# Kernel tuning notes

Measured on AMD Instinct MI355X. Metric: run time of the kernel, lower is better.

## Reference

```python
import jax, jax.numpy as jnp
import numpy as np

NUM_GRAPHS = 1024  # static number of segments for global_mean_pool


def setup_inputs() -> dict:
    key = jax.random.key(0)
    ks = jax.random.split(key, 16)
    N, E, F_IN, H = 100000, 1000000, 32, 64
    NUM_ATOM, NUM_ACT, L = 16, 8, 3
    s = 0.05
    x = jax.random.normal(ks[0], (N, F_IN), dtype=jnp.float32)
    edge_index = jax.random.randint(ks[1], (2, E), 0, N, dtype=jnp.int64)
    batch = jnp.sort(jax.random.randint(ks[2], (N,), 0, NUM_GRAPHS, dtype=jnp.int64))
    W_emb = jax.random.normal(ks[3], (F_IN, H), dtype=jnp.float32) * s
    b_emb = jnp.zeros((H,), dtype=jnp.float32)
    W_convs = jax.random.normal(ks[4], (L, H, H), dtype=jnp.float32) * s
    b_convs = jnp.zeros((L, H), dtype=jnp.float32)
    W_act = jax.random.normal(ks[5], (H, NUM_ACT), dtype=jnp.float32) * s
    b_act = jnp.zeros((NUM_ACT,), dtype=jnp.float32)
    W_tgt = jax.random.normal(ks[6], (H, 1), dtype=jnp.float32) * s
    b_tgt = jnp.zeros((1,), dtype=jnp.float32)
    W_atom = jax.random.normal(ks[7], (H, NUM_ATOM), dtype=jnp.float32) * s
    b_atom = jnp.zeros((NUM_ATOM,), dtype=jnp.float32)
    return {"x": x, "edge_index": edge_index, "batch": batch,
            "W_emb": W_emb, "b_emb": b_emb, "W_convs": W_convs, "b_convs": b_convs,
            "W_act": W_act, "b_act": b_act, "W_tgt": W_tgt, "b_tgt": b_tgt,
            "W_atom": W_atom, "b_atom": b_atom}


def reference(x, edge_index, batch, W_emb, b_emb, W_convs, b_convs,
              W_act, b_act, W_tgt, b_tgt, W_atom, b_atom):
    N = x.shape[0]
    # --- GCN normalization with self-loops (PyG GCNConv default) ---
    self_idx = jnp.arange(N, dtype=edge_index.dtype)
    src = jnp.concatenate([edge_index[0], self_idx])  # message source (row)
    dst = jnp.concatenate([edge_index[1], self_idx])  # aggregation target (col)
    ones_e = jnp.ones(src.shape[0], dtype=x.dtype)
    deg = jax.ops.segment_sum(ones_e, dst, num_segments=N)  # in-degree + self-loop
    dinv = jnp.where(deg > 0, jax.lax.rsqrt(deg), 0.0)
    norm = (dinv[src] * dinv[dst])[:, None]  # [E+N, 1]

    h = jax.nn.relu(x @ W_emb + b_emb)  # node embedding
    for i in range(W_convs.shape[0]):
        m = (h @ W_convs[i])[src] * norm            # gather + scale
        agg = jax.ops.segment_sum(m, dst, num_segments=N)  # scatter-add
        h = jax.nn.relu(agg + b_convs[i])

    # --- global mean pool over graphs ---
    cnt = jax.ops.segment_sum(jnp.ones(N, dtype=x.dtype), batch, num_segments=NUM_GRAPHS)
    pooled = jax.ops.segment_sum(h, batch, num_segments=NUM_GRAPHS)
    pooled = pooled / jnp.maximum(cnt, 1.0)[:, None]

    action_type_logits = pooled @ W_act + b_act            # [G, num_action_types]
    target_node_logits = (h @ W_tgt + b_tgt)[:, 0]         # [N]
    new_atom_type_logits = pooled @ W_atom + b_atom        # [G, num_atom_types]
    return (action_type_logits, target_node_logits, new_atom_type_logits, h)
```

## Files before the change

kernel.cpp:

```cpp
#include <hip/hip_runtime.h>
#include <hip/hip_fp16.h>

#define HD 64
#define FIN 32
#define NG 1024
#define STRIDE 64
#define SLOT0 4
#define DEGCAP 59
#define SH 72

#define BINW 128
#define NBMAX 1024
#define EPB 8192
#define BINCAP 2048

typedef _Float16 f16x8 __attribute__((ext_vector_type(8)));
typedef float f32x4 __attribute__((ext_vector_type(4)));
typedef int i32x4 __attribute__((ext_vector_type(4)));

__device__ __forceinline__ int fmap(int jt, int c) {
    return (jt < 2) ? (2 * c + jt) : (32 + 2 * c + (jt - 2));
}

__device__ __forceinline__ void nt_store_h2(__half2 v, __half2* p) {
    __builtin_nontemporal_store(*(int*)&v, (int*)p);
}

__global__ __launch_bounds__(256) void k_prep(const int* __restrict__ dst,
                                              int* __restrict__ blkHist,
                                              int E, int NBINS,
                                              __half2* __restrict__ BaZR,
                                              __half2* __restrict__ BbZR,
                                              const float* __restrict__ Wconv,
                                              __half* __restrict__ Wf, int wtotal,
                                              const float* __restrict__ Wemb,
                                              __half* __restrict__ Wef) {
    __shared__ int hist[NBMAX];
    int b = blockIdx.x, t = threadIdx.x;
    if (b < 48) {
        int tid = b * 256 + t;
        if (tid < wtotal) {
            int layer = tid >> 12;
            int r = tid & 4095;
            int frag = r >> 9, lane = (r >> 3) & 63, e = r & 7;
            int jt = frag >> 1, kh = frag & 1;
            int k = kh * 32 + (lane >> 4) * 8 + e;
            int n = fmap(jt, lane & 15);
            Wf[tid] = (_Float16)Wconv[(size_t)layer * 4096 + k * 64 + n];
        }
    } else if (b < 56) {
        int tid = (b - 48) * 256 + t;
        if (tid < 2048) {
            int jt = tid >> 9, lane = (tid >> 3) & 63, e = tid & 7;
            int k = (lane >> 4) * 8 + e;
            int n = fmap(jt, lane & 15);
            Wef[tid] = (_Float16)Wemb[k * HD + n];
        }
    } else if (b == 56) {
        __half2 z = __floats2half2_rn(0.f, 0.f);
        if (t < 32) BaZR[t] = z;
        else if (t < 64) BbZR[t - 32] = z;
    }
    int e0 = b * EPB;
    if (e0 < E) {
        for (int i = t; i < NBMAX; i += 256) hist[i] = 0;
        __syncthreads();
        int e1 = e0 + EPB; if (e1 > E) e1 = E;
        for (int e = e0 + t; e < e1; e += 256) atomicAdd(&hist[dst[e] >> 7], 1);
        __syncthreads();
        for (int i = t; i < NBINS; i += 256) blkHist[b * NBMAX + i] = hist[i];
    }
}

__global__ __launch_bounds__(256) void k_scanA(int* __restrict__ blkHist,
                                               int* __restrict__ binTot, int nb) {
    __shared__ int s[256];
    int i = blockIdx.x;
    int t = threadIdx.x;
    int x = (t < nb) ? blkHist[t * NBMAX + i] : 0;
    s[t] = x;
    __syncthreads();
    for (int off = 1; off < 256; off <<= 1) {
        int v = s[t];
        int u = (t >= off) ? s[t - off] : 0;
        __syncthreads();
        s[t] = v + u;
        __syncthreads();
    }
    if (t < nb) blkHist[t * NBMAX + i] = s[t] - x;
    if (t == 255) binTot[i] = s[255];
}

__global__ __launch_bounds__(256) void k_scatter(const int* __restrict__ src,
                                                 const int* __restrict__ dst,
                                                 const int* __restrict__ blkBase,
                                                 int* __restrict__ binned,
                                                 int E, int NBINS) {
    __shared__ int base[NBMAX];
    __shared__ int lpos[NBMAX];
    int b = blockIdx.x, t = threadIdx.x;
    for (int i = t; i < NBMAX; i += 256) {
        lpos[i] = 0;
        base[i] = (i < NBINS) ? blkBase[b * NBMAX + i] : 0;
    }
    __syncthreads();
    int e0 = b * EPB;
    int e1 = e0 + EPB; if (e1 > E) e1 = E;
    for (int e = e0 + t; e < e1; e += 256) {
        int d = dst[e];
        int bin = d >> 7;
        int off = base[bin] + atomicAdd(&lpos[bin], 1);
        if (off < BINCAP)
            binned[bin * BINCAP + off] = (src[e] << 7) | (d & (BINW - 1));
    }
}

__global__ __launch_bounds__(256) void k_csr(const int* __restrict__ binned,
                                             const int* __restrict__ binTot,
                                             int* __restrict__ col, int N) {
    __shared__ int img[BINW * 64];
    __shared__ int cnt[BINW];
    int b = blockIdx.x, t = threadIdx.x;
    for (int i = t; i < BINW; i += 256) cnt[i] = 0;
    __syncthreads();
    int s = b * BINCAP;
    int tot = binTot[b]; if (tot > BINCAP) tot = BINCAP;
    int e = s + tot;
    for (int i = s + t; i < e; i += 256) {
        int w = binned[i];
        int ld = w & (BINW - 1);
        int p = atomicAdd(&cnt[ld], 1);
        if (p < STRIDE - SLOT0) img[ld * 64 + SLOT0 + p] = (int)((unsigned)w >> 7);
    }
    __syncthreads();
    for (int i = t; i < BINW; i += 256) img[i * 64] = cnt[i];
    __syncthreads();
    int v0 = b * BINW;
    int* out = col + ((size_t)v0 << 6);
    for (int j = t; j < BINW * 16; j += 256) {
        int row = j >> 4, j16 = j & 15;
        int node = v0 + row;
        int deg = cnt[row]; if (deg > DEGCAP) deg = DEGCAP;
        bool keep = (j16 == 0) || (j16 <= ((deg + 3) >> 2));
        if (node < N && keep) {
            i32x4 val = *(i32x4*)&img[j * 4];
            __builtin_nontemporal_store(val, (i32x4*)(out + j * 4));
        }
    }
}

__device__ __forceinline__ void gemm_from_lds(const __half* hs, const float* dvs,
                                              const float4* __restrict__ Wf4,
                                              __half2* __restrict__ Bout,
                                              int node0, int N, int t) {
    int lane = t & 63;
    int wv = t >> 6;
    int lm = lane & 15, kq = lane >> 4;
    union U { float4 f; f16x8 h; };
    U a0, a1;
    const __half* hrow = hs + (size_t)(wv * 16 + lm) * SH;
    a0.f = *(const float4*)(hrow + kq * 8);
    a1.f = *(const float4*)(hrow + 32 + kq * 8);
    f32x4 acc[4];
#pragma unroll
    for (int jt = 0; jt < 4; jt++) acc[jt] = (f32x4){0.f, 0.f, 0.f, 0.f};
#pragma unroll
    for (int jt = 0; jt < 4; jt++) {
        U b0, b1;
        b0.f = Wf4[(jt * 2 + 0) * 64 + lane];
        b1.f = Wf4[(jt * 2 + 1) * 64 + lane];
        acc[jt] = __builtin_amdgcn_mfma_f32_16x16x32_f16(a0.h, b0.h, acc[jt], 0, 0, 0);
        acc[jt] = __builtin_amdgcn_mfma_f32_16x16x32_f16(a1.h, b1.h, acc[jt], 0, 0, 0);
    }
#pragma unroll
    for (int r = 0; r < 4; r++) {
        int lv = wv * 16 + kq * 4 + r;
        int v = node0 + lv;
        if (v < N) {
            float dv = dvs[lv];
            nt_store_h2(__floats2half2_rn(acc[0][r] * dv, acc[1][r] * dv),
                        Bout + (size_t)v * 32 + lm);
            nt_store_h2(__floats2half2_rn(acc[2][r] * dv, acc[3][r] * dv),
                        Bout + (size_t)v * 32 + 16 + lm);
        }
    }
}

__global__ __launch_bounds__(256) void k_emb_gemm0(const float* __restrict__ x,
                                                   const float4* __restrict__ Wef4,
                                                   const float* __restrict__ bemb,
                                                   const int* __restrict__ col,
                                                   const float4* __restrict__ Wf0,
                                                   __half2* __restrict__ Bout, int N) {
    __shared__ __half hs[64 * SH];
    __shared__ float dvs[64];
    int t = threadIdx.x;
    int lane = t & 63;
    int wv = t >> 6;
    int node0 = blockIdx.x * 64;
    int nodew = node0 + wv * 16;
    int m = lane & 15, kq = lane >> 4;

    int vm = nodew + m;
    if (vm > N - 1) vm = N - 1;
    const float4* xr = (const float4*)(x + (size_t)vm * FIN + kq * 8);
    float4 xa = xr[0], xb = xr[1];
    f16x8 a;
    a[0] = (_Float16)xa.x; a[1] = (_Float16)xa.y; a[2] = (_Float16)xa.z; a[3] = (_Float16)xa.w;
    a[4] = (_Float16)xb.x; a[5] = (_Float16)xb.y; a[6] = (_Float16)xb.z; a[7] = (_Float16)xb.w;

    union U { float4 f; f16x8 h; };
    f32x4 acc[4];
#pragma unroll
    for (int jt = 0; jt < 4; jt++) {
        U b; b.f = Wef4[jt * 64 + lane];
        acc[jt] = (f32x4){0.f, 0.f, 0.f, 0.f};
        acc[jt] = __builtin_amdgcn_mfma_f32_16x16x32_f16(a, b.h, acc[jt], 0, 0, 0);
    }
    float b01x = bemb[2 * m], b01y = bemb[2 * m + 1];
    float b23x = bemb[32 + 2 * m], b23y = bemb[32 + 2 * m + 1];
    __half2 z = __floats2half2_rn(0.f, 0.f);
#pragma unroll
    for (int r = 0; r < 4; r++) {
        int lv = wv * 16 + kq * 4 + r;
        int v = node0 + lv;
        __half2 p01 = z, p23 = z;
        if (v < N) {
            p01 = __floats2half2_rn(fmaxf(acc[0][r] + b01x, 0.f),
                                    fmaxf(acc[1][r] + b01y, 0.f));
            p23 = __floats2half2_rn(fmaxf(acc[2][r] + b23x, 0.f),
                                    fmaxf(acc[3][r] + b23y, 0.f));
        }
        *(__half2*)(hs + (size_t)lv * SH + 2 * m) = p01;
        *(__half2*)(hs + (size_t)lv * SH + 32 + 2 * m) = p23;
        if (m == 0)
            dvs[lv] = (v < N) ? rsqrtf((float)(col[(size_t)v << 6] + 1)) : 1.f;
    }
    __syncthreads();
    gemm_from_lds(hs, dvs, Wf0, Bout, node0, N, t);
}

__global__ __launch_bounds__(256) void k_layer(const __half2* __restrict__ Bin,
                                               const int* __restrict__ col,
                                               const float* __restrict__ bias,
                                               const float4* __restrict__ Wnext,
                                               __half2* __restrict__ Bout,
                                               int N, int ZR) {
    __shared__ __half hs[64 * SH];
    __shared__ float dvs[64];
    int t = threadIdx.x;
    int lane = t & 63;
    int wv = t >> 6;
    int node0 = blockIdx.x * 64;
    int q = lane >> 4, p = lane & 15;
    float4 b4 = *(const float4*)(bias + 4 * p);

#pragma unroll
    for (int pass = 0; pass < 4; pass++) {
        int lv = wv * 16 + pass * 4 + q;
        int v = node0 + lv;
        int vc = (v < N) ? v : 0;
        const int* bucket = col + ((size_t)vc << 6);
        int degraw = bucket[0];
        int deg = degraw > DEGCAP ? DEGCAP : degraw;
        int dmax = deg;
        dmax = max(dmax, __shfl_xor(dmax, 16, 64));
        dmax = max(dmax, __shfl_xor(dmax, 32, 64));
        int rounds = (dmax + 4) >> 2;

        float2 a0 = make_float2(0.f, 0.f), a1 = make_float2(0.f, 0.f);
        for (int rd = 0; rd < rounds; rd++) {
            int4 iq = *(const int4*)(bucket + SLOT0 + rd * 4);
            int idx[4] = {iq.x, iq.y, iq.z, iq.w};
#pragma unroll
            for (int r = 0; r < 4; r++) {
                int i = rd * 4 + r;
                idx[r] = (i < deg) ? idx[r] : ((i == deg) ? vc : ZR);
            }
            float2 raw[4];
#pragma unroll
            for (int r = 0; r < 4; r++)
                raw[r] = *(const float2*)(Bin + (size_t)idx[r] * 32 + p * 2);
#pragma unroll
            for (int r = 0; r < 4; r++) {
                float2 f0 = __half22float2(((const __half2*)&raw[r])[0]);
                float2 f1 = __half22float2(((const __half2*)&raw[r])[1]);
                a0.x += f0.x; a0.y += f0.y; a1.x += f1.x; a1.y += f1.y;
            }
        }
        float dv = rsqrtf((float)(degraw + 1));
        float r0 = fmaxf(dv * a0.x + b4.x, 0.f);
        float r1 = fmaxf(dv * a0.y + b4.y, 0.f);
        float r2 = fmaxf(dv * a1.x + b4.z, 0.f);
        float r3 = fmaxf(dv * a1.y + b4.w, 0.f);
        if (v >= N) { r0 = r1 = r2 = r3 = 0.f; dv = 1.f; }
        __half* hrow = hs + (size_t)lv * SH + 4 * p;
        *(__half2*)(hrow) = __floats2half2_rn(r0, r1);
        *(__half2*)(hrow + 2) = __floats2half2_rn(r2, r3);
        if (p == 0) dvs[lv] = dv;
    }
    __syncthreads();
    gemm_from_lds(hs, dvs, Wnext, Bout, node0, N, t);
}

__global__ __launch_bounds__(256) void k_gather_last(const __half2* __restrict__ Bin,
                                                     const int* __restrict__ col,
                                                     const float* __restrict__ bias,
                                                     float* __restrict__ hout,
                                                     const float* __restrict__ Wtgt,
                                                     const float* __restrict__ btgt,
                                                     float* __restrict__ tgt,
                                                     int N, int ZR) {
    int t = threadIdx.x;
    int lane = t & 63;
    int wv = t >> 6;
    int q = lane >> 4, p = lane & 15;
    int v = blockIdx.x * 16 + wv * 4 + q;
    if (v >= N) return;

    const int* bucket = col + ((size_t)v << 6);
    int degraw = bucket[0];
    int deg = degraw > DEGCAP ? DEGCAP : degraw;
    int dmax = deg;
    dmax = max(dmax, __shfl_xor(dmax, 16, 64));
    dmax = max(dmax, __shfl_xor(dmax, 32, 64));
    int rounds = (dmax + 4) >> 2;

    float2 a0 = make_float2(0.f, 0.f), a1 = make_float2(0.f, 0.f);
    for (int rd = 0; rd < rounds; rd++) {
        int4 iq = *(const int4*)(bucket + SLOT0 + rd * 4);
        int idx[4] = {iq.x, iq.y, iq.z, iq.w};
#pragma unroll
        for (int r = 0; r < 4; r++) {
            int i = rd * 4 + r;
            idx[r] = (i < deg) ? idx[r] : ((i == deg) ? v : ZR);
        }
        float2 raw[4];
#pragma unroll
        for (int r = 0; r < 4; r++)
            raw[r] = *(const float2*)(Bin + (size_t)idx[r] * 32 + p * 2);
#pragma unroll
        for (int r = 0; r < 4; r++) {
            float2 f0 = __half22float2(((const __half2*)&raw[r])[0]);
            float2 f1 = __half22float2(((const __half2*)&raw[r])[1]);
            a0.x += f0.x; a0.y += f0.y; a1.x += f1.x; a1.y += f1.y;
        }
    }
    float dv = rsqrtf((float)(degraw + 1));
    float4 b4 = *(const float4*)(bias + 4 * p);
    float r0 = fmaxf(dv * a0.x + b4.x, 0.f);
    float r1 = fmaxf(dv * a0.y + b4.y, 0.f);
    float r2 = fmaxf(dv * a1.x + b4.z, 0.f);
    float r3 = fmaxf(dv * a1.y + b4.w, 0.f);
    f32x4 o = (f32x4){r0, r1, r2, r3};
    __builtin_nontemporal_store(o, (f32x4*)(hout + (size_t)v * HD + 4 * p));
    float4 w4 = *(const float4*)(Wtgt + 4 * p);
    float pp = r0 * w4.x + r1 * w4.y + r2 * w4.z + r3 * w4.w;
    pp += __shfl_xor(pp, 1, 64); pp += __shfl_xor(pp, 2, 64);
    pp += __shfl_xor(pp, 4, 64); pp += __shfl_xor(pp, 8, 64);
    if (p == 0) __builtin_nontemporal_store(pp + btgt[0], tgt + v);
}

__global__ __launch_bounds__(256) void k_pool(const float* __restrict__ h,
                                              const int* __restrict__ batch,
                                              const float* __restrict__ Wact,
                                              const float* __restrict__ bact,
                                              const float* __restrict__ Watom,
                                              const float* __restrict__ batom,
                                              float* __restrict__ out_act,
                                              float* __restrict__ out_atom, int N) {
    int g = blockIdx.x;
    int t = threadIdx.x;
    int q = t >> 4, p = t & 15;
    int lo = 0, hi = N;
    while (lo < hi) { int mid = (lo + hi) >> 1; if (batch[mid] < g) lo = mid + 1; else hi = mid; }
    int s = lo;
    hi = N;
    while (lo < hi) { int mid = (lo + hi) >> 1; if (batch[mid] < g + 1) lo = mid + 1; else hi = mid; }
    int e2 = lo;
    float4 acc = make_float4(0.f, 0.f, 0.f, 0.f);
    for (int v = s + q; v < e2; v += 16) {
        float4 c = *(const float4*)(h + (size_t)v * HD + p * 4);
        acc.x += c.x; acc.y += c.y; acc.z += c.z; acc.w += c.w;
    }
    __shared__ float4 part[16][16];
    part[q][p] = acc;
    __syncthreads();
    __shared__ float pl[HD];
    if (t < 16) {
        float4 tot = part[0][t];
#pragma unroll
        for (int k = 1; k < 16; k++) {
            float4 c = part[k][t];
            tot.x += c.x; tot.y += c.y; tot.z += c.z; tot.w += c.w;
        }
        float cnt = fmaxf((float)(e2 - s), 1.f);
        pl[t * 4 + 0] = tot.x / cnt; pl[t * 4 + 1] = tot.y / cnt;
        pl[t * 4 + 2] = tot.z / cnt; pl[t * 4 + 3] = tot.w / cnt;
    }
    __syncthreads();
    if (t < 8) {
        float a = bact[t];
#pragma unroll
        for (int k = 0; k < HD; k++) a += pl[k] * Wact[k * 8 + t];
        out_act[g * 8 + t] = a;
    }
    if (t < 16) {
        float a = batom[t];
#pragma unroll
        for (int k = 0; k < HD; k++) a += pl[k] * Watom[k * 16 + t];
        out_atom[g * 16 + t] = a;
    }
}

extern "C" void kernel_launch(void* const* d_in, const int* in_sizes, int n_in,
                              void* d_out, int out_size, void* d_ws, size_t ws_size,
                              hipStream_t stream) {
    const float* x     = (const float*)d_in[0];
    const int*   ei    = (const int*)d_in[1];
    const int*   batch = (const int*)d_in[2];
    const float* Wemb  = (const float*)d_in[3];
    const float* bemb  = (const float*)d_in[4];
    const float* Wconv = (const float*)d_in[5];
    const float* bconv = (const float*)d_in[6];
    const float* Wact  = (const float*)d_in[7];
    const float* bact  = (const float*)d_in[8];
    const float* Wtgt  = (const float*)d_in[9];
    const float* btgt  = (const float*)d_in[10];
    const float* Watom = (const float*)d_in[11];
    const float* batom = (const float*)d_in[12];

    const int N = in_sizes[0] / FIN;
    const int E = in_sizes[1] / 2;
    const int L = in_sizes[5] / (HD * HD);
    const int Npad = (N + 63) & ~63;
    const int ZR = Npad;

    int*     col = (int*)d_ws;
    __half2* Ba  = (__half2*)(col + ((size_t)N << 6));
    __half2* Bb  = Ba + (size_t)(Npad + 64) * 32;
    __half*  Wf  = (__half*)(Bb + (size_t)(Npad + 64) * 32);
    __half*  Wef = Wf + (size_t)L * 4096;

    int* binned  = (int*)Bb;
    int* blkHist = (int*)((char*)Bb + (8u << 20));
    int* binTot  = (int*)((char*)Bb + (9u << 20));

    const int* srcA = ei;
    const int* dstA = ei + E;

    float* out_act  = (float*)d_out;
    float* out_tgt  = out_act + (size_t)NG * 8;
    float* out_atom = out_tgt + N;
    float* out_h    = out_atom + (size_t)NG * 16;

    const int nbG = (N + 63) / 64;
    const int nbLast = (N + 15) / 16;
    const int wtotal = L * 4096;
    const int nbF1 = (E + EPB - 1) / EPB;
    const int NBINS = (N + BINW - 1) / BINW;
    const int nbPrep = nbF1 > 57 ? nbF1 : 57;

    k_prep<<<nbPrep, 256, 0, stream>>>(dstA, blkHist, E, NBINS,
                                       Ba + (size_t)ZR * 32, Bb + (size_t)ZR * 32,
                                       Wconv, Wf, wtotal, Wemb, Wef);
    k_scanA<<<NBINS, 256, 0, stream>>>(blkHist, binTot, nbF1);
    k_scatter<<<nbF1, 256, 0, stream>>>(srcA, dstA, blkHist, binned, E, NBINS);
    k_csr<<<NBINS, 256, 0, stream>>>(binned, binTot, col, N);
    k_emb_gemm0<<<nbG, 256, 0, stream>>>(x, (const float4*)Wef, bemb, col,
                                         (const float4*)Wf, Ba, N);

    __half2* cur = Ba;
    __half2* nxt = Bb;
    for (int l = 0; l < L - 1; ++l) {
        k_layer<<<nbG, 256, 0, stream>>>(cur, col, bconv + l * HD,
                                         (const float4*)(Wf + (size_t)(l + 1) * 4096),
                                         nxt, N, ZR);
        __half2* tmp = cur; cur = nxt; nxt = tmp;
    }
    k_gather_last<<<nbLast, 256, 0, stream>>>(cur, col, bconv + (size_t)(L - 1) * HD,
                                              out_h, Wtgt, btgt, out_tgt, N, ZR);
    k_pool<<<NG, 256, 0, stream>>>(out_h, batch, Wact, bact, Watom, batom,
                                   out_act, out_atom, N);
}
```

Baseline: 238.2 us.

## Fuse CSR build kernels into one cooperative kernel with grid syncs

Merges the histogram/prep, bin scan, scatter and per-bin CSR kernels into a single cooperatively launched kernel that separates the phases with grid-wide syncs. Edges per block are halved, so the histogram and scatter phases run on more blocks. The binTot buffer is moved so it does not overlap the now larger blkHist array. This removes three kernel launches and their gaps, at the cost of grid-sync overhead and the requirement that all blocks (the larger of the bin count and histogram-plus-prep blocks) be resident at once.

```diff
diff --git a/kernel.cpp b/kernel.cpp
--- a/kernel.cpp
+++ b/kernel.cpp
@@ -1,5 +1,8 @@
 #include <hip/hip_runtime.h>
 #include <hip/hip_fp16.h>
+#include <hip/hip_cooperative_groups.h>
+
+namespace cg = cooperative_groups;
 
 #define HD 64
 #define FIN 32
@@ -11,8 +14,9 @@
 
 #define BINW 128
 #define NBMAX 1024
-#define EPB 8192
+#define EPB 4096
 #define BINCAP 2048
+#define SWZB 57
 
 typedef _Float16 f16x8 __attribute__((ext_vector_type(8)));
 typedef float f32x4 __attribute__((ext_vector_type(4)));
@@ -26,125 +30,124 @@
     __builtin_nontemporal_store(*(int*)&v, (int*)p);
 }
 
-__global__ __launch_bounds__(256) void k_prep(const int* __restrict__ dst,
-                                              int* __restrict__ blkHist,
-                                              int E, int NBINS,
-                                              __half2* __restrict__ BaZR,
-                                              __half2* __restrict__ BbZR,
-                                              const float* __restrict__ Wconv,
-                                              __half* __restrict__ Wf, int wtotal,
-                                              const float* __restrict__ Wemb,
-                                              __half* __restrict__ Wef) {
-    __shared__ int hist[NBMAX];
+__global__ __launch_bounds__(256) void k_build(const int* __restrict__ src,
+                                               const int* __restrict__ dst,
+                                               int* __restrict__ blkHist,
+                                               int* __restrict__ binTot,
+                                               int* __restrict__ binned,
+                                               int* __restrict__ col,
+                                               int E, int N, int NBINS, int nbH,
+                                               __half2* __restrict__ BaZR,
+                                               __half2* __restrict__ BbZR,
+                                               const float* __restrict__ Wconv,
+                                               __half* __restrict__ Wf, int wtotal,
+                                               const float* __restrict__ Wemb,
+                                               __half* __restrict__ Wef) {
+    __shared__ int smem[BINW * 64 + BINW];
+    cg::grid_group grid = cg::this_grid();
     int b = blockIdx.x, t = threadIdx.x;
-    if (b < 48) {
-        int tid = b * 256 + t;
-        if (tid < wtotal) {
-            int layer = tid >> 12;
-            int r = tid & 4095;
-            int frag = r >> 9, lane = (r >> 3) & 63, e = r & 7;
-            int jt = frag >> 1, kh = frag & 1;
-            int k = kh * 32 + (lane >> 4) * 8 + e;
-            int n = fmap(jt, lane & 15);
-            Wf[tid] = (_Float16)Wconv[(size_t)layer * 4096 + k * 64 + n];
-        }
-    } else if (b < 56) {
-        int tid = (b - 48) * 256 + t;
-        if (tid < 2048) {
-            int jt = tid >> 9, lane = (tid >> 3) & 63, e = tid & 7;
-            int k = (lane >> 4) * 8 + e;
-            int n = fmap(jt, lane & 15);
-            Wef[tid] = (_Float16)Wemb[k * HD + n];
-        }
-    } else if (b == 56) {
-        __half2 z = __floats2half2_rn(0.f, 0.f);
-        if (t < 32) BaZR[t] = z;
-        else if (t < 64) BbZR[t - 32] = z;
-    }
-    int e0 = b * EPB;
-    if (e0 < E) {
-        for (int i = t; i < NBMAX; i += 256) hist[i] = 0;
-        __syncthreads();
+
+    if (b < nbH) {
+        for (int i = t; i < NBMAX; i += 256) smem[i] = 0;
+        __syncthreads();
+        int e0 = b * EPB;
         int e1 = e0 + EPB; if (e1 > E) e1 = E;
-        for (int e = e0 + t; e < e1; e += 256) atomicAdd(&hist[dst[e] >> 7], 1);
-        __syncthreads();
-        for (int i = t; i < NBINS; i += 256) blkHist[b * NBMAX + i] = hist[i];
-    }
-}
-
-__global__ __launch_bounds__(256) void k_scanA(int* __restrict__ blkHist,
-                                               int* __restrict__ binTot, int nb) {
-    __shared__ int s[256];
-    int i = blockIdx.x;
-    int t = threadIdx.x;
-    int x = (t < nb) ? blkHist[t * NBMAX + i] : 0;
-    s[t] = x;
-    __syncthreads();
-    for (int off = 1; off < 256; off <<= 1) {
-        int v = s[t];
-        int u = (t >= off) ? s[t - off] : 0;
-        __syncthreads();
-        s[t] = v + u;
-        __syncthreads();
-    }
-    if (t < nb) blkHist[t * NBMAX + i] = s[t] - x;
-    if (t == 255) binTot[i] = s[255];
-}
-
-__global__ __launch_bounds__(256) void k_scatter(const int* __restrict__ src,
-                                                 const int* __restrict__ dst,
-                                                 const int* __restrict__ blkBase,
-                                                 int* __restrict__ binned,
-                                                 int E, int NBINS) {
-    __shared__ int base[NBMAX];
-    __shared__ int lpos[NBMAX];
-    int b = blockIdx.x, t = threadIdx.x;
-    for (int i = t; i < NBMAX; i += 256) {
-        lpos[i] = 0;
-        base[i] = (i < NBINS) ? blkBase[b * NBMAX + i] : 0;
-    }
-    __syncthreads();
-    int e0 = b * EPB;
-    int e1 = e0 + EPB; if (e1 > E) e1 = E;
-    for (int e = e0 + t; e < e1; e += 256) {
-        int d = dst[e];
-        int bin = d >> 7;
-        int off = base[bin] + atomicAdd(&lpos[bin], 1);
-        if (off < BINCAP)
-            binned[bin * BINCAP + off] = (src[e] << 7) | (d & (BINW - 1));
-    }
-}
-
-__global__ __launch_bounds__(256) void k_csr(const int* __restrict__ binned,
-                                             const int* __restrict__ binTot,
-                                             int* __restrict__ col, int N) {
-    __shared__ int img[BINW * 64];
-    __shared__ int cnt[BINW];
-    int b = blockIdx.x, t = threadIdx.x;
-    for (int i = t; i < BINW; i += 256) cnt[i] = 0;
-    __syncthreads();
-    int s = b * BINCAP;
-    int tot = binTot[b]; if (tot > BINCAP) tot = BINCAP;
-    int e = s + tot;
-    for (int i = s + t; i < e; i += 256) {
-        int w = binned[i];
-        int ld = w & (BINW - 1);
-        int p = atomicAdd(&cnt[ld], 1);
-        if (p < STRIDE - SLOT0) img[ld * 64 + SLOT0 + p] = (int)((unsigned)w >> 7);
-    }
-    __syncthreads();
-    for (int i = t; i < BINW; i += 256) img[i * 64] = cnt[i];
-    __syncthreads();
-    int v0 = b * BINW;
-    int* out = col + ((size_t)v0 << 6);
-    for (int j = t; j < BINW * 16; j += 256) {
-        int row = j >> 4, j16 = j & 15;
-        int node = v0 + row;
-        int deg = cnt[row]; if (deg > DEGCAP) deg = DEGCAP;
-        bool keep = (j16 == 0) || (j16 <= ((deg + 3) >> 2));
-        if (node < N && keep) {
-            i32x4 val = *(i32x4*)&img[j * 4];
-            __builtin_nontemporal_store(val, (i32x4*)(out + j * 4));
+        for (int e = e0 + t; e < e1; e += 256) atomicAdd(&smem[dst[e] >> 7], 1);
+        __syncthreads();
+        for (int i = t; i < NBINS; i += 256) blkHist[b * NBMAX + i] = smem[i];
+    } else {
+        int bb = b - nbH;
+        if (bb < 48) {
+            int tid = bb * 256 + t;
+            if (tid < wtotal) {
+                int layer = tid >> 12;
+                int r = tid & 4095;
+                int frag = r >> 9, lane = (r >> 3) & 63, e = r & 7;
+                int jt = frag >> 1, kh = frag & 1;
+                int k = kh * 32 + (lane >> 4) * 8 + e;
+                int n = fmap(jt, lane & 15);
+                Wf[tid] = (_Float16)Wconv[(size_t)layer * 4096 + k * 64 + n];
+            }
+        } else if (bb < 56) {
+            int tid = (bb - 48) * 256 + t;
+            if (tid < 2048) {
+                int jt = tid >> 9, lane = (tid >> 3) & 63, e = tid & 7;
+                int k = (lane >> 4) * 8 + e;
+                int n = fmap(jt, lane & 15);
+                Wef[tid] = (_Float16)Wemb[k * HD + n];
+            }
+        } else if (bb == 56) {
+            __half2 z = __floats2half2_rn(0.f, 0.f);
+            if (t < 32) BaZR[t] = z;
+            else if (t < 64) BbZR[t - 32] = z;
+        }
+    }
+    grid.sync();
+
+    if (b < NBINS) {
+        int x = (t < nbH) ? blkHist[t * NBMAX + b] : 0;
+        smem[t] = x;
+        __syncthreads();
+        for (int off = 1; off < 256; off <<= 1) {
+            int v = smem[t];
+            int u = (t >= off) ? smem[t - off] : 0;
+            __syncthreads();
+            smem[t] = v + u;
+            __syncthreads();
+        }
+        if (t < nbH) blkHist[t * NBMAX + b] = smem[t] - x;
+        if (t == 255) binTot[b] = smem[255];
+    }
+    grid.sync();
+
+    if (b < nbH) {
+        int* base = smem;
+        int* lpos = smem + NBMAX;
+        for (int i = t; i < NBMAX; i += 256) {
+            lpos[i] = 0;
+            base[i] = (i < NBINS) ? blkHist[b * NBMAX + i] : 0;
+        }
+        __syncthreads();
+        int e0 = b * EPB;
+        int e1 = e0 + EPB; if (e1 > E) e1 = E;
+        for (int e = e0 + t; e < e1; e += 256) {
+            int d = dst[e];
+            int bin = d >> 7;
+            int off = base[bin] + atomicAdd(&lpos[bin], 1);
+            if (off < BINCAP)
+                binned[bin * BINCAP + off] = (src[e] << 7) | (d & (BINW - 1));
+        }
+    }
+    grid.sync();
+
+    if (b < NBINS) {
+        int* img = smem;
+        int* cnt = smem + BINW * 64;
+        for (int i = t; i < BINW; i += 256) cnt[i] = 0;
+        __syncthreads();
+        int s0 = b * BINCAP;
+        int tot = binTot[b]; if (tot > BINCAP) tot = BINCAP;
+        int e = s0 + tot;
+        for (int i = s0 + t; i < e; i += 256) {
+            int w = binned[i];
+            int ld = w & (BINW - 1);
+            int p = atomicAdd(&cnt[ld], 1);
+            if (p < STRIDE - SLOT0) img[ld * 64 + SLOT0 + p] = (int)((unsigned)w >> 7);
+        }
+        __syncthreads();
+        for (int i = t; i < BINW; i += 256) img[i * 64] = cnt[i];
+        __syncthreads();
+        int v0 = b * BINW;
+        int* out = col + ((size_t)v0 << 6);
+        for (int j = t; j < BINW * 16; j += 256) {
+            int row = j >> 4, j16 = j & 15;
+            int node = v0 + row;
+            int deg = cnt[row]; if (deg > DEGCAP) deg = DEGCAP;
+            bool keep = (j16 == 0) || (j16 <= ((deg + 3) >> 2));
+            if (node < N && keep) {
+                i32x4 val = *(i32x4*)&img[j * 4];
+                __builtin_nontemporal_store(val, (i32x4*)(out + j * 4));
+            }
         }
     }
 }
@@ -444,7 +447,7 @@
 
     int* binned  = (int*)Bb;
     int* blkHist = (int*)((char*)Bb + (8u << 20));
-    int* binTot  = (int*)((char*)Bb + (9u << 20));
+    int* binTot  = (int*)((char*)Bb + (9u << 20) + (512u << 10));
 
     const int* srcA = ei;
     const int* dstA = ei + E;
@@ -457,16 +460,27 @@
     const int nbG = (N + 63) / 64;
     const int nbLast = (N + 15) / 16;
     const int wtotal = L * 4096;
-    const int nbF1 = (E + EPB - 1) / EPB;
+    const int nbH = (E + EPB - 1) / EPB;
     const int NBINS = (N + BINW - 1) / BINW;
-    const int nbPrep = nbF1 > 57 ? nbF1 : 57;
-
-    k_prep<<<nbPrep, 256, 0, stream>>>(dstA, blkHist, E, NBINS,
-                                       Ba + (size_t)ZR * 32, Bb + (size_t)ZR * 32,
-                                       Wconv, Wf, wtotal, Wemb, Wef);
-    k_scanA<<<NBINS, 256, 0, stream>>>(blkHist, binTot, nbF1);
-    k_scatter<<<nbF1, 256, 0, stream>>>(srcA, dstA, blkHist, binned, E, NBINS);
-    k_csr<<<NBINS, 256, 0, stream>>>(binned, binTot, col, N);
+    int nbBuild = NBINS > (nbH + SWZB) ? NBINS : (nbH + SWZB);
+
+    __half2* BaZRp = Ba + (size_t)ZR * 32;
+    __half2* BbZRp = Bb + (size_t)ZR * 32;
+    int E_ = E, N_ = N, NBINS_ = NBINS, nbH_ = nbH, wtotal_ = wtotal;
+    const int* srcA_ = srcA; const int* dstA_ = dstA;
+    int* blkHist_ = blkHist; int* binTot_ = binTot; int* binned_ = binned; int* col_ = col;
+    const float* Wconv_ = Wconv; __half* Wf_ = Wf;
+    const float* Wemb_ = Wemb;  __half* Wef_ = Wef;
+    void* args[] = {
+        (void*)&srcA_, (void*)&dstA_, (void*)&blkHist_, (void*)&binTot_,
+        (void*)&binned_, (void*)&col_,
+        (void*)&E_, (void*)&N_, (void*)&NBINS_, (void*)&nbH_,
+        (void*)&BaZRp, (void*)&BbZRp,
+        (void*)&Wconv_, (void*)&Wf_, (void*)&wtotal_,
+        (void*)&Wemb_, (void*)&Wef_
+    };
+    hipLaunchCooperativeKernel((void*)k_build, dim3(nbBuild), dim3(256), args, 0, stream);
+
     k_emb_gemm0<<<nbG, 256, 0, stream>>>(x, (const float4*)Wef, bemb, col,
                                          (const float4*)Wf, Ba, N);
 
```

Result: slower. 516.8 us (+117.0%).
